# Optimization experiments

Hardware: AMD Instinct MI355X
Metric: run time of the kernel (lower is better)

The kernel has to match this reference:

```python
import jax, jax.numpy as jnp
import numpy as np

MAX_DIS = 4  # max_displacement == pad_size


def setup_inputs() -> dict:
    key = jax.random.key(0)
    k1, k2 = jax.random.split(key)
    in1 = jax.random.normal(k1, (2, 64, 32, 32, 32), dtype=jnp.float32)
    in2 = jax.random.normal(k2, (2, 64, 32, 32, 32), dtype=jnp.float32)
    return {"in1": in1, "in2": in2}


def _corr3d(in1, in2, max_dis):
    # in1, in2: [B, C, H, W, D]
    B, C, H, W, D = in1.shape
    K = 2 * max_dis + 1
    pad = ((0, 0), (0, 0), (max_dis, max_dis), (max_dis, max_dis), (max_dis, max_dis))
    in2_pad = jnp.pad(in2, pad)  # [B, C, H+2m, W+2m, D+2m]
    # gather index for the depth axis: all K shifted windows at once
    idx_d = jnp.arange(K)[:, None] + jnp.arange(D)[None, :]  # [K, D]
    outs = []
    # loop over the (dy, dx) shift grid (fixed 9x9 structural loop);
    # the dz shifts and the channel reduction are fully vectorized.
    for dy in range(K):
        for dx in range(K):
            s = in2_pad[:, :, dy:dy + H, dx:dx + W, :]          # [B, C, H, W, D+2m]
            w = s[..., idx_d]                                   # [B, C, H, W, K, D]
            # sum over channels -> K correlation channels (dz inner)
            outs.append(jnp.einsum('bchwkd,bchwd->bkhwd', w, in1))
    # channel order matches torch: n = dy*K*K + dx*K + dz
    return jnp.concatenate(outs, axis=1)  # [B, K^3, H, W, D]


def reference(in1, in2):
    return _corr3d(in1, in2, MAX_DIS)
```

## Files before the change

kernel.cpp:

```cpp
#include <hip/hip_runtime.h>

typedef __fp16 h2 __attribute__((ext_vector_type(2)));
typedef __fp16 h8 __attribute__((ext_vector_type(8)));
typedef float f4 __attribute__((ext_vector_type(4)));

namespace {
constexpr int JSTR = 72;
constexpr int JN = 48;
constexpr int COLH = JN * JSTR;
}

__global__ __launch_bounds__(256, 4) void corr3d_mfma(
    const float* __restrict__ in1, const float* __restrict__ in2,
    float* __restrict__ out)
{
  __shared__ __align__(16) __fp16 colbuf[2][COLH];
  __shared__ __align__(16) float obuf[2 * 9 * 32];

  const int tid = threadIdx.x;
  const int blk = ((blockIdx.x & 7) << 7) | (blockIdx.x >> 3);
  const int b = blk >> 9;
  const int h = (blk >> 4) & 31;
  const int w0 = (blk & 15) << 1;

  const int lane = tid & 63;
  const int wv = tid >> 6;
  const int jb = (wv == 0) ? 0 : (wv == 3) ? 32 : 16;
  const int db = (wv >= 2) ? 16 : 0;
  const int l15 = lane & 15;
  const int lhi = lane >> 4;

  const float* in1b = in1 + ((size_t)b << 21);
  const float* in2b = in2 + ((size_t)b << 21);

  for (int i = tid; i < 1152; i += 256) {
    const int bu = i / 576;
    const int r = i - bu * 576;
    const int jrow = r / 36;
    const int cc = r - jrow * 36;
    const int j = (jrow < 4) ? jrow : jrow + 32;
    h2 z = {(__fp16)0.f, (__fp16)0.f};
    *(h2*)&colbuf[bu][j * JSTR + cc * 2] = z;
  }

  const int sd = tid & 31;
  const int scq = tid >> 5;

  auto stage = [&](const float* src, bool valid, __fp16* dst) {
#pragma unroll
    for (int it = 0; it < 4; ++it) {
      const int cp = scq + (it << 3);
      h2 v = {(__fp16)0.f, (__fp16)0.f};
      if (valid) {
        const float x = src[((size_t)(2 * cp) << 15) + sd];
        const float y = src[((size_t)(2 * cp + 1) << 15) + sd];
        v = __builtin_amdgcn_cvt_pkrtz(x, y);
      }
      *(h2*)&dst[(4 + sd) * JSTR + 2 * cp] = v;
    }
  };

  h8 bfr[2][2];
#pragma unroll
  for (int pos = 0; pos < 2; ++pos) {
    __syncthreads();
    stage(in1b + (h << 10) + ((w0 + pos) << 5), true, colbuf[0]);
    __syncthreads();
#pragma unroll
    for (int ch = 0; ch < 2; ++ch)
      bfr[pos][ch] =
          *(const h8*)&colbuf[0][(4 + db + l15) * JSTR + ch * 32 + (lhi << 3)];
  }
  __syncthreads();
  {
    const int hp = h - 4, wp = w0 - 4;
    const bool valid = ((unsigned)hp < 32u) && ((unsigned)wp < 32u);
    stage(in2b + (hp << 10) + (wp << 5), valid, colbuf[0]);
  }
  __syncthreads();

  int boff[4];
  unsigned bmask = 0;
#pragma unroll
  for (int r = 0; r < 4; ++r) {
    const int m = (lhi << 2) + r;
    const int dz = jb + m - db - l15;
    if ((unsigned)dz < 9u) bmask |= 1u << r;
    boff[r] = dz * 32 + db + l15;
  }

  for (int ci = 0; ci < 90; ++ci) {
    if (ci + 1 < 90) {
      const int cn = ci + 1;
      const int hcn = cn / 10;
      const int wcn = cn - hcn * 10;
      const int hp = h - 4 + hcn;
      const int wp = w0 - 4 + wcn;
      const bool valid = ((unsigned)hp < 32u) && ((unsigned)wp < 32u);
      stage(in2b + (hp << 10) + (wp << 5), valid, colbuf[cn & 1]);
    }
    const int hc = ci / 10;
    const int wc = ci - hc * 10;
    const bool serve[2] = {wc <= 8, wc >= 1};

    const __fp16* cb = colbuf[ci & 1];
    const h8 a0 = *(const h8*)&cb[(jb + l15) * JSTR + (lhi << 3)];
    const h8 a1 = *(const h8*)&cb[(jb + l15) * JSTR + 32 + (lhi << 3)];
#pragma unroll
    for (int pos = 0; pos < 2; ++pos) {
      if (serve[pos]) {
        f4 acc = {0.f, 0.f, 0.f, 0.f};
        acc = __builtin_amdgcn_mfma_f32_16x16x32_f16(a0, bfr[pos][0], acc, 0, 0, 0);
        acc = __builtin_amdgcn_mfma_f32_16x16x32_f16(a1, bfr[pos][1], acc, 0, 0, 0);
#pragma unroll
        for (int r = 0; r < 4; ++r)
          if (bmask & (1u << r)) obuf[pos * 288 + boff[r]] = acc[r];
      }
    }
    __syncthreads();
    if (tid < 144) {
      const int pos = tid >= 72;
      const int rr = tid - pos * 72;
      const int dz = rr >> 3;
      const int q = rr & 7;
      if (serve[pos]) {
        const f4 v = *(const f4*)&obuf[pos * 288 + dz * 32 + (q << 2)];
        const size_t ch = (size_t)(b * 729 + (hc * 9 + (wc - pos)) * 9 + dz);
        f4* dstp = (f4*)(out + (ch << 15) + (h << 10) + ((w0 + pos) << 5) + (q << 2));
        __builtin_nontemporal_store(v, dstp);
      }
    }
    __syncthreads();
  }
}

extern "C" void kernel_launch(void* const* d_in, const int* in_sizes, int n_in,
                              void* d_out, int out_size, void* d_ws, size_t ws_size,
                              hipStream_t stream) {
  const float* in1 = (const float*)d_in[0];
  const float* in2 = (const float*)d_in[1];
  float* out = (float*)d_out;
  corr3d_mfma<<<dim3(1024), dim3(256), 0, stream>>>(in1, in2, out);
}
```

Measured before the change: 280.8 us.

## Double-buffer output staging and defer global loads to overlap with MFMA

Double-buffers the shared output staging buffer so each iteration writes out the previous iteration's results. This removes one of the two block barriers per iteration. The next column's global loads are now issued into registers at the top of the loop and converted and stored to LDS after the MFMA work, so load latency overlaps compute. A tail block flushes the last iteration's output. The cost is extra registers and LDS.

```diff
diff --git a/kernel.cpp b/kernel.cpp
--- a/kernel.cpp
+++ b/kernel.cpp
@@ -15,7 +15,7 @@
     float* __restrict__ out)
 {
   __shared__ __align__(16) __fp16 colbuf[2][COLH];
-  __shared__ __align__(16) float obuf[2 * 9 * 32];
+  __shared__ __align__(16) float obuf[2][2 * 9 * 32];
 
   const int tid = threadIdx.x;
   const int blk = ((blockIdx.x & 7) << 7) | (blockIdx.x >> 3);
@@ -90,20 +90,32 @@
   }
 
   for (int ci = 0; ci < 90; ++ci) {
+    float lx[4], ly[4];
+    bool nvalid = false;
     if (ci + 1 < 90) {
       const int cn = ci + 1;
       const int hcn = cn / 10;
       const int wcn = cn - hcn * 10;
       const int hp = h - 4 + hcn;
       const int wp = w0 - 4 + wcn;
-      const bool valid = ((unsigned)hp < 32u) && ((unsigned)wp < 32u);
-      stage(in2b + (hp << 10) + (wp << 5), valid, colbuf[cn & 1]);
+      nvalid = ((unsigned)hp < 32u) && ((unsigned)wp < 32u);
+      if (nvalid) {
+        const float* src = in2b + (hp << 10) + (wp << 5);
+#pragma unroll
+        for (int it = 0; it < 4; ++it) {
+          const int cp = scq + (it << 3);
+          lx[it] = src[((size_t)(2 * cp) << 15) + sd];
+          ly[it] = src[((size_t)(2 * cp + 1) << 15) + sd];
+        }
+      }
     }
+
     const int hc = ci / 10;
     const int wc = ci - hc * 10;
     const bool serve[2] = {wc <= 8, wc >= 1};
 
     const __fp16* cb = colbuf[ci & 1];
+    float* ob = obuf[ci & 1];
     const h8 a0 = *(const h8*)&cb[(jb + l15) * JSTR + (lhi << 3)];
     const h8 a1 = *(const h8*)&cb[(jb + l15) * JSTR + 32 + (lhi << 3)];
 #pragma unroll
@@ -114,23 +126,48 @@
         acc = __builtin_amdgcn_mfma_f32_16x16x32_f16(a1, bfr[pos][1], acc, 0, 0, 0);
 #pragma unroll
         for (int r = 0; r < 4; ++r)
-          if (bmask & (1u << r)) obuf[pos * 288 + boff[r]] = acc[r];
+          if (bmask & (1u << r)) ob[pos * 288 + boff[r]] = acc[r];
       }
     }
-    __syncthreads();
-    if (tid < 144) {
+
+    if (ci > 0 && tid < 144) {
+      const int cprev = ci - 1;
+      const int hcp = cprev / 10;
+      const int wcp = cprev - hcp * 10;
       const int pos = tid >= 72;
       const int rr = tid - pos * 72;
       const int dz = rr >> 3;
       const int q = rr & 7;
-      if (serve[pos]) {
-        const f4 v = *(const f4*)&obuf[pos * 288 + dz * 32 + (q << 2)];
-        const size_t ch = (size_t)(b * 729 + (hc * 9 + (wc - pos)) * 9 + dz);
+      const bool sv = pos ? (wcp >= 1) : (wcp <= 8);
+      if (sv) {
+        const f4 v = *(const f4*)&obuf[cprev & 1][pos * 288 + dz * 32 + (q << 2)];
+        const size_t ch = (size_t)(b * 729 + (hcp * 9 + (wcp - pos)) * 9 + dz);
         f4* dstp = (f4*)(out + (ch << 15) + (h << 10) + ((w0 + pos) << 5) + (q << 2));
         __builtin_nontemporal_store(v, dstp);
       }
     }
+
+    if (ci + 1 < 90) {
+#pragma unroll
+      for (int it = 0; it < 4; ++it) {
+        const int cp = scq + (it << 3);
+        h2 v = {(__fp16)0.f, (__fp16)0.f};
+        if (nvalid) v = __builtin_amdgcn_cvt_pkrtz(lx[it], ly[it]);
+        *(h2*)&colbuf[(ci + 1) & 1][(4 + sd) * JSTR + 2 * cp] = v;
+      }
+    }
+
     __syncthreads();
+  }
+
+  if (tid >= 72 && tid < 144) {
+    const int rr = tid - 72;
+    const int dz = rr >> 3;
+    const int q = rr & 7;
+    const f4 v = *(const f4*)&obuf[1][288 + dz * 32 + (q << 2)];
+    const size_t ch = (size_t)(b * 729 + (8 * 9 + 8) * 9 + dz);
+    f4* dstp = (f4*)(out + (ch << 15) + (h << 10) + ((w0 + 1) << 5) + (q << 2));
+    __builtin_nontemporal_store(v, dstp);
   }
 }
 
```

After: 279.9 us. Within noise of the previous version (-0.3%).
